# Optimization experiments

Measured on AMD Instinct MI355X. Metric: run time of the kernel, lower is better.

## Reference

```python
import jax, jax.numpy as jnp
import numpy as np

N, DIN, H, OUT = 2048, 128, 64, 7


def setup_inputs() -> dict:
    key = jax.random.key(0)
    ks = jax.random.split(key, 24)

    def lin(k, out_d, in_d):
        kw, kb = jax.random.split(k)
        s = 1.0 / np.sqrt(in_d)
        W = jax.random.uniform(kw, (out_d, in_d), minval=-s, maxval=s, dtype=jnp.float32)
        b = jax.random.uniform(kb, (out_d,), minval=-s, maxval=s, dtype=jnp.float32)
        return W, b

    x = jax.random.normal(ks[0], (N, DIN), dtype=jnp.float32)
    A = jax.random.uniform(ks[1], (N, N), dtype=jnp.float32)
    W1, b1 = lin(ks[2], H, DIN)
    WF1, bF1 = lin(ks[3], H, H)
    WF2, bF2 = lin(ks[4], H, H)
    WT1, bT1 = lin(ks[5], H, H)
    WT2, bT2 = lin(ks[6], H, H)
    WC1, bC1 = lin(ks[7], H, H)
    WC2, bC2 = lin(ks[8], H, H)
    Wa, ba = lin(ks[9], H, H)
    q = jax.random.normal(ks[10], (H,), dtype=jnp.float32)
    W2, b2 = lin(ks[11], OUT, H)
    return dict(x=x, A=A, k=4, W1=W1, b1=b1, WF1=WF1, bF1=bF1, WF2=WF2, bF2=bF2,
                WT1=WT1, bT1=bT1, WT2=WT2, bT2=bT2, WC1=WC1, bC1=bC1, WC2=WC2,
                bC2=bC2, Wa=Wa, ba=ba, q=q, W2=W2, b2=b2)


def leaky(x):
    return jnp.where(x > 0, x, 0.1 * x)


def laplacian(A):
    # D^{-1/2} A D^{-1/2} with diagonal D of (rowsum + 1e-10)
    d = (jnp.sum(A, -1) + 1e-10) ** -0.5
    return A * d[:, None] * d[None, :]


def cos_sim(x):
    n = jnp.sqrt(jnp.sum(x * x, -1, keepdims=True))
    s = x / n + 1e-10  # note: +1e-10 AFTER the division, as in the source
    return s @ s.T


def heat(x):
    # exp(-0.5 * sum_d ((x_i - x_j)^2 + 1e-10)); gram trick, same math as
    # the [d, N, N] broadcasted version in the source.
    sq = jnp.sum(x * x, -1)
    dist = sq[:, None] + sq[None, :] - 2.0 * (x @ x.T) + x.shape[-1] * 1e-10
    return jnp.exp(-0.5 * dist)


def l2_norm_rows(x):
    m = jnp.sqrt(jnp.mean(x * x, -1)) + 1e-10
    return x / m[:, None]


def hsic(x1, x2):
    n = x1.shape[-2]
    K1 = x1 @ x1.T
    K2 = x2 @ x2.T
    Rm = jnp.eye(n, dtype=x1.dtype) - jnp.ones((n, n), dtype=x1.dtype) / n
    P = Rm @ K1 @ Rm  # [N, N]
    # mean(I * (P @ K2)) * n^2/(n-1)^2 = trace(P @ K2)/(n-1)^2; K2 symmetric
    return jnp.sum(P * K2) / (n - 1) ** 2


def gnn(z, Ad, W, b):
    return leaky((Ad @ z) @ W.T + b)


def reference(x, A, k, W1, b1, WF1, bF1, WF2, bF2, WT1, bT1, WT2, bT2,
              WC1, bC1, WC2, bC2, Wa, ba, q, W2, b2):
    h = leaky(x @ W1.T + b1)                       # [N, H]
    At = laplacian(A)
    Hh = heat(h)                                    # [N, N]
    rank = jnp.argsort(jnp.argsort(-Hh, axis=-1), axis=-1)  # double-argsort rank
    mask = (rank < k).astype(h.dtype)
    Af = laplacian(cos_sim(h) * mask)
    zf = gnn(gnn(h, Af, WF1, bF1), Af, WF2, bF2)
    zt = gnn(gnn(h, At, WT1, bT1), At, WT2, bT2)
    zcf = gnn(gnn(h, Af, WC1, bC1), Af, WC2, bC2)
    zct = gnn(gnn(h, At, WC1, bC1), At, WC2, bC2)
    Lcf = l2_norm_rows(zcf)
    Lct = l2_norm_rows(zct)
    Lc = jnp.mean((Lcf @ Lcf.T - Lct @ Lct.T) ** 2)
    Ld = hsic(zt, zct) + hsic(zf, zcf)
    zc = (zcf + zct) / 2
    z = jnp.stack([zf, zt, zc], axis=-2)            # [N, 3, H]
    a = jax.nn.softmax(jnp.tanh(z @ Wa.T + ba) @ q, axis=-1)  # [N, 3]
    zagg = jnp.einsum('nkd,nk->nd', z, a)           # [N, H]
    out = zagg @ W2.T + b2                          # [N, OUT]
    return (out, Lc, Ld)
```

## Files before the change

### kernel.cpp

```cpp
#include <hip/hip_runtime.h>
#include <stdint.h>

#define N 2048
#define DIN 128
#define H 64
#define OUTD 7
#define RS 32
#define S1 8
#define S2 8

#define Z_ZT  0
#define Z_ZCT 64
#define Z_ZF  128
#define Z_ZCF 192
#define Z_LCF 256
#define Z_LCT 320

typedef short bf16x8 __attribute__((ext_vector_type(8)));
typedef float floatx4 __attribute__((ext_vector_type(4)));

__device__ __forceinline__ float leaky(float x){ return x > 0.f ? x : 0.1f*x; }

__device__ __forceinline__ unsigned short f2bf(float f){
  unsigned int u = __float_as_uint(f);
  u = u + 0x7FFFu + ((u >> 16) & 1u);
  return (unsigned short)(u >> 16);
}

__device__ __forceinline__ float waveRedSum(float v){
  #pragma unroll
  for (int o = 32; o > 0; o >>= 1) v += __shfl_xor(v, o, 64);
  return v;
}

__device__ __forceinline__ unsigned long long shflx64(unsigned long long v, int m){
  unsigned int lo = (unsigned int)v, hi = (unsigned int)(v >> 32);
  lo = (unsigned int)__shfl_xor((int)lo, m, 64);
  hi = (unsigned int)__shfl_xor((int)hi, m, 64);
  return ((unsigned long long)hi << 32) | lo;
}

__global__ void k_prep(const float* __restrict__ A, float* __restrict__ dA,
                       unsigned short* __restrict__ Abf){
  int i = blockIdx.x;
  const float4* row = (const float4*)(A + (size_t)i * N);
  unsigned short* ob = Abf + (size_t)i * N;
  float s = 0.f;
  #pragma unroll
  for (int it = 0; it < 2; it++){
    int u = threadIdx.x + it*256;
    float4 v = row[u];
    s += v.x + v.y + v.z + v.w;
    ushort4 o;
    o.x = f2bf(v.x); o.y = f2bf(v.y); o.z = f2bf(v.z); o.w = f2bf(v.w);
    *(ushort4*)&ob[u*4] = o;
  }
  __shared__ float red[4];
  s = waveRedSum(s);
  int wid = threadIdx.x >> 6, lane = threadIdx.x & 63;
  if (lane == 0) red[wid] = s;
  __syncthreads();
  if (threadIdx.x == 0){
    float t = red[0] + red[1] + red[2] + red[3];
    dA[i] = 1.0f / sqrtf(t + 1e-10f);
  }
}

__global__ void k_h(const float* __restrict__ x, const float* __restrict__ W1,
                    const float* __restrict__ b1, const float* __restrict__ dA,
                    float* __restrict__ h, unsigned short* __restrict__ hsT,
                    float* __restrict__ sq, float* __restrict__ hsum){
  int i = blockIdx.x, t = threadIdx.x;
  __shared__ float xr[DIN];
  xr[t]      = x[(size_t)i*DIN + t];
  xr[t + 64] = x[(size_t)i*DIN + t + 64];
  __syncthreads();
  float acc = b1[t];
  const float4* w  = (const float4*)(W1 + (size_t)t*DIN);
  const float4* xv = (const float4*)xr;
  #pragma unroll
  for (int c = 0; c < DIN/4; c++){
    float4 a = xv[c], b = w[c];
    acc += a.x*b.x + a.y*b.y + a.z*b.z + a.w*b.w;
  }
  float hv = leaky(acc);
  h[(size_t)i*H + t] = hv;
  hsT[(size_t)t*N + i] = f2bf(dA[i]*hv);
  float s2 = waveRedSum(hv*hv);
  float s1 = waveRedSum(hv);
  if (t == 0){ sq[i] = s2; hsum[i] = s1; }
}

__global__ __launch_bounds__(256) void k_gram(const float* __restrict__ h,
                                              float* __restrict__ DOT){
  __shared__ float at[32][132];
  __shared__ float bt[32][132];
  int bi = blockIdx.x, bj = blockIdx.y;
  int tid = threadIdx.x;
  int rg = tid >> 4, cg = tid & 15;
  float acc[8][8] = {};
  for (int kc = 0; kc < 64; kc += 32){
    for (int u = tid; u < 1024; u += 256){
      int row = u >> 3, k4 = u & 7;
      float4 v = *(const float4*)(h + (size_t)(bi*128 + row)*H + kc + k4*4);
      at[k4*4+0][row] = v.x; at[k4*4+1][row] = v.y;
      at[k4*4+2][row] = v.z; at[k4*4+3][row] = v.w;
    }
    for (int u = tid; u < 1024; u += 256){
      int row = u >> 3, k4 = u & 7;
      float4 v = *(const float4*)(h + (size_t)(bj*128 + row)*H + kc + k4*4);
      bt[k4*4+0][row] = v.x; bt[k4*4+1][row] = v.y;
      bt[k4*4+2][row] = v.z; bt[k4*4+3][row] = v.w;
    }
    __syncthreads();
    for (int k = 0; k < 32; k++){
      float a[8], b[8];
      *(float4*)&a[0] = *(const float4*)&at[k][rg*8];
      *(float4*)&a[4] = *(const float4*)&at[k][rg*8+4];
      *(float4*)&b[0] = *(const float4*)&bt[k][cg*8];
      *(float4*)&b[4] = *(const float4*)&bt[k][cg*8+4];
      #pragma unroll
      for (int ii = 0; ii < 8; ii++)
        #pragma unroll
        for (int jj = 0; jj < 8; jj++)
          acc[ii][jj] += a[ii]*b[jj];
    }
    __syncthreads();
  }
  #pragma unroll
  for (int ii = 0; ii < 8; ii++){
    int r = bi*128 + rg*8 + ii;
    float* out = DOT + (size_t)r*N + bj*128 + cg*8;
    *(float4*)(out)   = make_float4(acc[ii][0], acc[ii][1], acc[ii][2], acc[ii][3]);
    *(float4*)(out+4) = make_float4(acc[ii][4], acc[ii][5], acc[ii][6], acc[ii][7]);
  }
}

__global__ __launch_bounds__(256) void k_topk(const float* __restrict__ DOT,
      const float* __restrict__ sq, const float* __restrict__ hsum,
      int* __restrict__ nidx, float* __restrict__ ncos, float* __restrict__ df){
  int i = blockIdx.x, tid = threadIdx.x;
  __shared__ unsigned long long cand[1024];
  const float4* row = (const float4*)(DOT + (size_t)i * N);
  const float4* sq4 = (const float4*)sq;
  unsigned long long best[4] = {~0ULL, ~0ULL, ~0ULL, ~0ULL};
  #pragma unroll
  for (int blk = 0; blk < 2; blk++){
    int u = tid + blk*256;
    float4 d = row[u];
    float4 s = sq4[u];
    float kv[4] = { s.x - 2.f*d.x, s.y - 2.f*d.y, s.z - 2.f*d.z, s.w - 2.f*d.w };
    #pragma unroll
    for (int e = 0; e < 4; e++){
      unsigned int j = (unsigned int)(u*4 + e);
      unsigned int uk = __float_as_uint(kv[e]);
      uk = (uk & 0x80000000u) ? ~uk : (uk | 0x80000000u);
      unsigned long long c = ((unsigned long long)uk << 32) | j;
      if (c < best[3]){
        best[3] = c;
        unsigned long long t0;
        if (best[3] < best[2]){ t0 = best[2]; best[2] = best[3]; best[3] = t0; }
        if (best[2] < best[1]){ t0 = best[1]; best[1] = best[2]; best[2] = t0; }
        if (best[1] < best[0]){ t0 = best[0]; best[0] = best[1]; best[1] = t0; }
      }
    }
  }
  #pragma unroll
  for (int e = 0; e < 4; e++) cand[e*256 + tid] = best[e];
  __syncthreads();
  if (tid < 64){
    unsigned long long loc[16];
    #pragma unroll
    for (int e = 0; e < 16; e++) loc[e] = cand[e*64 + tid];
    unsigned long long w0=~0ULL, w1=~0ULL, w2=~0ULL, w3=~0ULL;
    #pragma unroll
    for (int r = 0; r < 4; r++){
      unsigned long long m = loc[0];
      #pragma unroll
      for (int e = 1; e < 16; e++) m = (loc[e] < m) ? loc[e] : m;
      unsigned long long g = m;
      #pragma unroll
      for (int o = 32; o > 0; o >>= 1){
        unsigned long long other = shflx64(g, o);
        if (other < g) g = other;
      }
      #pragma unroll
      for (int e = 0; e < 16; e++) if (loc[e] == g) loc[e] = ~0ULL;
      if (r == 0) w0 = g; else if (r == 1) w1 = g; else if (r == 2) w2 = g; else w3 = g;
    }
    float myc = 0.f;
    if (tid < 4){
      unsigned long long w = (tid==0) ? w0 : (tid==1) ? w1 : (tid==2) ? w2 : w3;
      unsigned int j = (unsigned int)w;
      unsigned int uk = (unsigned int)(w >> 32);
      float key = (uk & 0x80000000u) ? __uint_as_float(uk ^ 0x80000000u)
                                     : __uint_as_float(~uk);
      float sqj = sq[j];
      float dot = (sqj - key) * 0.5f;
      float hni = sqrtf(sq[i]), hnj = sqrtf(sqj);
      float cosv = dot/(hni*hnj)
                 + 1e-10f*(hsum[i]/hni + hsum[j]/hnj)
                 + 64.0f*1e-20f;
      nidx[i*4 + tid] = (int)j;
      ncos[i*4 + tid] = cosv;
      myc = cosv;
    }
    myc += __shfl_xor(myc, 1, 64);
    myc += __shfl_xor(myc, 2, 64);
    if (tid == 0) df[i] = 1.f / sqrtf(myc + 1e-10f);
  }
}

template<int BN>
__global__ __launch_bounds__(256) void k_mgemm(
    const unsigned short* __restrict__ Abf, const unsigned short* __restrict__ BtG,
    float* __restrict__ Cp, int KC){
  __shared__ __align__(16) unsigned short Asl[64][72];
  __shared__ __align__(16) unsigned short Bsl[BN][72];
  int m0 = blockIdx.x * 64, kbase = blockIdx.y * KC;
  int tid = threadIdx.x;
  int w = tid >> 6, lane = tid & 63;
  int quad = lane >> 4, ml = lane & 15;
  floatx4 acc[BN/16];
  #pragma unroll
  for (int ct = 0; ct < BN/16; ct++) acc[ct] = (floatx4){0.f,0.f,0.f,0.f};

  for (int kc = 0; kc < KC; kc += 64){
    int kb = kbase + kc;
    #pragma unroll
    for (int u = tid; u < 512; u += 256){
      int r = u >> 3, s = u & 7;
      *(uint4*)&Asl[r][s*8] = *(const uint4*)(Abf + ((size_t)(m0+r) << 11) + kb + s*8);
    }
    #pragma unroll
    for (int u = tid; u < BN*8; u += 256){
      int n = u >> 3, s = u & 7;
      *(uint4*)&Bsl[n][s*8] = *(const uint4*)(BtG + ((size_t)n << 11) + kb + s*8);
    }
    __syncthreads();
    #pragma unroll
    for (int k0 = 0; k0 < 64; k0 += 32){
      bf16x8 af = *(const bf16x8*)&Asl[16*w + ml][k0 + quad*8];
      #pragma unroll
      for (int ct = 0; ct < BN/16; ct++){
        bf16x8 bfr = *(const bf16x8*)&Bsl[16*ct + ml][k0 + quad*8];
        acc[ct] = __builtin_amdgcn_mfma_f32_16x16x32_bf16(af, bfr, acc[ct], 0, 0, 0);
      }
    }
    __syncthreads();
  }
  float* C = Cp + (size_t)blockIdx.y * (N * BN);
  #pragma unroll
  for (int ct = 0; ct < BN/16; ct++)
    #pragma unroll
    for (int r = 0; r < 4; r++){
      int row = m0 + 16*w + quad*4 + r;
      C[(size_t)row*BN + 16*ct + ml] = acc[ct][r];
    }
}

__global__ void k_z1(const float* __restrict__ h, const int* __restrict__ nidx,
                     const float* __restrict__ ncos, const float* __restrict__ df,
                     const float* __restrict__ Y1p, const float* __restrict__ dA,
                     const float* __restrict__ WF1, const float* __restrict__ bF1,
                     const float* __restrict__ WC1, const float* __restrict__ bC1,
                     const float* __restrict__ WT1, const float* __restrict__ bT1,
                     float* __restrict__ z1f, float* __restrict__ z1cf,
                     unsigned short* __restrict__ ZsT){
  int i = blockIdx.x, tid = threadIdx.x, w = tid >> 6, t = tid & 63;
  __shared__ float vu[2][H];
  if (w == 0){
    int j0 = nidx[i*4], j1 = nidx[i*4+1], j2 = nidx[i*4+2], j3 = nidx[i*4+3];
    float di = df[i];
    float w0 = ncos[i*4]  *di*df[j0];
    float w1 = ncos[i*4+1]*di*df[j1];
    float w2 = ncos[i*4+2]*di*df[j2];
    float w3 = ncos[i*4+3]*di*df[j3];
    vu[0][t] = w0*h[(size_t)j0*H+t] + w1*h[(size_t)j1*H+t]
             + w2*h[(size_t)j2*H+t] + w3*h[(size_t)j3*H+t];
  } else {
    float y = 0.f;
    #pragma unroll
    for (int p = 0; p < S1; p++) y += Y1p[(size_t)p*(N*H) + (size_t)i*H + t];
    vu[1][t] = dA[i] * y;
  }
  __syncthreads();
  const float* Wx = (w == 0) ? WF1 : WT1;
  const float* bx = (w == 0) ? bF1 : bT1;
  float a1 = bx[t], a2 = bC1[t];
  const float4* wx = (const float4*)(Wx + (size_t)t*H);
  const float4* wc = (const float4*)(WC1 + (size_t)t*H);
  const float4* vv = (const float4*)vu[w];
  #pragma unroll
  for (int c = 0; c < 16; c++){
    float4 x = vv[c], f = wx[c], g = wc[c];
    a1 += x.x*f.x + x.y*f.y + x.z*f.z + x.w*f.w;
    a2 += x.x*g.x + x.y*g.y + x.z*g.z + x.w*g.w;
  }
  if (w == 0){
    z1f [(size_t)i*H+t] = leaky(a1);
    z1cf[(size_t)i*H+t] = leaky(a2);
  } else {
    float di = dA[i];
    ZsT[(size_t)t*N + i]        = f2bf(di*leaky(a1));
    ZsT[(size_t)(64+t)*N + i]   = f2bf(di*leaky(a2));
  }
}

__global__ void k_z2o(const float* __restrict__ z1f, const float* __restrict__ z1cf,
                      const int* __restrict__ nidx, const float* __restrict__ ncos,
                      const float* __restrict__ df,
                      const float* __restrict__ Y2p, const float* __restrict__ dA,
                      const float* __restrict__ WF2, const float* __restrict__ bF2,
                      const float* __restrict__ WC2, const float* __restrict__ bC2,
                      const float* __restrict__ WT2, const float* __restrict__ bT2,
                      const float* __restrict__ Wa, const float* __restrict__ ba,
                      const float* __restrict__ q, const float* __restrict__ W2,
                      const float* __restrict__ b2,
                      float* __restrict__ Z6, float* __restrict__ out){
  int i = blockIdx.x, tid = threadIdx.x, w = tid >> 6, t = tid & 63;
  __shared__ float v[4][H];
  __shared__ float zsh[4][H];
  __shared__ float esh[3];
  __shared__ float zagg[H];
  if (w < 2){
    int j0 = nidx[i*4], j1 = nidx[i*4+1], j2 = nidx[i*4+2], j3 = nidx[i*4+3];
    float di = df[i];
    float w0 = ncos[i*4]  *di*df[j0];
    float w1 = ncos[i*4+1]*di*df[j1];
    float w2 = ncos[i*4+2]*di*df[j2];
    float w3 = ncos[i*4+3]*di*df[j3];
    const float* src = (w == 0) ? z1f : z1cf;
    v[w][t] = w0*src[(size_t)j0*H+t] + w1*src[(size_t)j1*H+t]
            + w2*src[(size_t)j2*H+t] + w3*src[(size_t)j3*H+t];
  } else {
    int off = (w == 2) ? 0 : 64;
    float y = 0.f;
    #pragma unroll
    for (int p = 0; p < S2; p++) y += Y2p[(size_t)p*(N*128) + (size_t)i*128 + off + t];
    v[w][t] = dA[i] * y;
  }
  __syncthreads();
  const float* WM = (w == 0) ? WF2 : (w == 2) ? WT2 : WC2;
  const float* bb = (w == 0) ? bF2 : (w == 2) ? bT2 : bC2;
  float a = bb[t];
  const float4* wm = (const float4*)(WM + (size_t)t*H);
  const float4* vv = (const float4*)v[w];
  #pragma unroll
  for (int c = 0; c < 16; c++){
    float4 x = vv[c], f = wm[c];
    a += x.x*f.x + x.y*f.y + x.z*f.z + x.w*f.w;
  }
  float val = leaky(a);
  float* zr = Z6 + (size_t)i*384;
  if (w == 0){
    zr[Z_ZF + t] = val;  zsh[0][t] = val;
  } else if (w == 2){
    zr[Z_ZT + t] = val;  zsh[1][t] = val;
  } else {
    int cf = (w == 1);
    zr[(cf ? Z_ZCF : Z_ZCT) + t] = val;
    zsh[cf ? 2 : 3][t] = val;
    float s = waveRedSum(val*val);
    float m = sqrtf(s*(1.f/64.f)) + 1e-10f;
    zr[(cf ? Z_LCF : Z_LCT) + t] = val/m;
  }
  __syncthreads();
  if (w < 3){
    float aa = ba[t];
    const float4* wa = (const float4*)(Wa + (size_t)t*H);
    const float4* z0 = (const float4*)zsh[w == 0 ? 0 : (w == 1 ? 1 : 2)];
    const float4* z3 = (const float4*)zsh[3];
    #pragma unroll
    for (int c = 0; c < 16; c++){
      float4 wv = wa[c];
      float4 zv = z0[c];
      if (w == 2){
        float4 z2v = z3[c];
        zv.x = 0.5f*(zv.x + z2v.x); zv.y = 0.5f*(zv.y + z2v.y);
        zv.z = 0.5f*(zv.z + z2v.z); zv.w = 0.5f*(zv.w + z2v.w);
      }
      aa += zv.x*wv.x + zv.y*wv.y + zv.z*wv.z + zv.w*wv.w;
    }
    float wk = tanhf(aa);
    float e = waveRedSum(wk*q[t]);
    if (t == 0) esh[w] = e;
  }
  __syncthreads();
  if (w == 3){
    float e0 = esh[0], e1 = esh[1], e2 = esh[2];
    float mx = fmaxf(e0, fmaxf(e1, e2));
    float x0 = expf(e0-mx), x1 = expf(e1-mx), x2 = expf(e2-mx);
    float inv = 1.f/(x0+x1+x2);
    float a0 = x0*inv, a1 = x1*inv, a2 = x2*inv;
    zagg[t] = a0*zsh[0][t] + a1*zsh[1][t] + a2*0.5f*(zsh[2][t] + zsh[3][t]);
    if (t < OUTD){
      float acc2 = b2[t];
      const float* w2r = W2 + (size_t)t*H;
      #pragma unroll
      for (int c = 0; c < H; c++) acc2 += zagg[c]*w2r[c];
      out[(size_t)i*OUTD + t] = acc2;
    }
  }
}

__global__ __launch_bounds__(256) void k_reduce(const float* __restrict__ Z6,
                                                float* __restrict__ redP,
                                                float* __restrict__ colP){
  __shared__ float sa[64][68];
  __shared__ float sb[64][68];
  int p = blockIdx.x >> 5;
  int s = blockIdx.x & 31;
  int tid = threadIdx.x;
  const int aoffT[5] = {Z_ZT,  Z_ZF,  Z_LCF, Z_LCF, Z_LCT};
  const int boffT[5] = {Z_ZCT, Z_ZCF, Z_LCF, Z_LCT, Z_LCT};
  int aoff = aoffT[p], boff = boffT[p];
  int r0 = s * 64;
  {
    int row = tid >> 4, c4 = (tid & 15) * 4;
    #pragma unroll
    for (int rr = 0; rr < 64; rr += 16){
      const float* zr = Z6 + (size_t)(r0 + row + rr) * 384;
      *(float4*)&sa[row + rr][c4] = *(const float4*)&zr[aoff + c4];
      *(float4*)&sb[row + rr][c4] = *(const float4*)&zr[boff + c4];
    }
  }
  __syncthreads();
  int rg = tid >> 4, cg = tid & 15;
  float acc[4][4] = {};
  #pragma unroll 8
  for (int k = 0; k < 64; k++){
    float a[4], b[4];
    *(float4*)a = *(const float4*)&sa[k][rg*4];
    *(float4*)b = *(const float4*)&sb[k][cg*4];
    #pragma unroll
    for (int ii = 0; ii < 4; ii++)
      #pragma unroll
      for (int jj = 0; jj < 4; jj++)
        acc[ii][jj] += a[ii]*b[jj];
  }
  float* rp = redP + (size_t)blockIdx.x * 4096;
  #pragma unroll
  for (int ii = 0; ii < 4; ii++)
    *(float4*)&rp[(rg*4+ii)*64 + cg*4] =
      make_float4(acc[ii][0], acc[ii][1], acc[ii][2], acc[ii][3]);
  if (p < 2 && tid < 128){
    int t = tid & 63;
    float csum = 0.f;
    if (tid < 64){
      #pragma unroll 16
      for (int r = 0; r < 64; r++) csum += sa[r][t];
    } else {
      #pragma unroll 16
      for (int r = 0; r < 64; r++) csum += sb[r][t];
    }
    colP[((size_t)p*RS + s)*128 + tid] = csum;
  }
}

__global__ void k_combine(const float* __restrict__ redP,
                          const float* __restrict__ colP,
                          float* __restrict__ red){
  int idx = blockIdx.x*256 + threadIdx.x;
  if (idx < 20480){
    int p = idx >> 12, i = idx & 4095;
    float sum = 0.f;
    #pragma unroll 8
    for (int s = 0; s < RS; s++) sum += redP[((size_t)p*RS + s)*4096 + i];
    red[idx] = sum;
  } else if (idx < 20736){
    int j = idx - 20480;
    int p = j >> 7, rem = j & 127;
    float sum = 0.f;
    #pragma unroll 8
    for (int s = 0; s < RS; s++) sum += colP[((size_t)p*RS + s)*128 + rem];
    red[idx] = sum;
  }
}

__global__ void k_final(const float* __restrict__ red, float* __restrict__ out2){
  int tid = threadIdx.x;
  const float* Stc = red;
  const float* Sfc = red + 4096;
  const float* Cff = red + 8192;
  const float* Cft = red + 12288;
  const float* Ctt = red + 16384;
  const float* cst = red + 20480;
  const float* csct= red + 20544;
  const float* csf = red + 20608;
  const float* cscf= red + 20672;
  float sCff=0, sCft=0, sCtt=0, sM1=0, sM2=0;
  for (int u = tid*16; u < tid*16+16; u++){
    int d = u >> 6, e = u & 63;
    float m1 = Stc[u] - cst[d]*csct[e]*(1.f/2048.f);
    float m2 = Sfc[u] - csf[d]*cscf[e]*(1.f/2048.f);
    sM1 += m1*m1; sM2 += m2*m2;
    float cf = Cff[u], cx = Cft[u], ct = Ctt[u];
    sCff += cf*cf; sCft += cx*cx; sCtt += ct*ct;
  }
  __shared__ float rd[5][4];
  sCff = waveRedSum(sCff); sCft = waveRedSum(sCft); sCtt = waveRedSum(sCtt);
  sM1 = waveRedSum(sM1);   sM2 = waveRedSum(sM2);
  int w = tid >> 6, lane = tid & 63;
  if (lane == 0){ rd[0][w]=sCff; rd[1][w]=sCft; rd[2][w]=sCtt; rd[3][w]=sM1; rd[4][w]=sM2; }
  __syncthreads();
  if (tid == 0){
    float A0 = rd[0][0]+rd[0][1]+rd[0][2]+rd[0][3];
    float A1 = rd[1][0]+rd[1][1]+rd[1][2]+rd[1][3];
    float A2 = rd[2][0]+rd[2][1]+rd[2][2]+rd[2][3];
    float M1 = rd[3][0]+rd[3][1]+rd[3][2]+rd[3][3];
    float M2 = rd[4][0]+rd[4][1]+rd[4][2]+rd[4][3];
    out2[0] = (A0 - 2.f*A1 + A2) * (1.f/(2048.f*2048.f));
    out2[1] = (M1 + M2) * (1.f/(2047.f*2047.f));
  }
}

extern "C" void kernel_launch(void* const* d_in, const int* in_sizes, int n_in,
                              void* d_out, int out_size, void* d_ws, size_t ws_size,
                              hipStream_t stream) {
  const float* x   = (const float*)d_in[0];
  const float* A   = (const float*)d_in[1];
  const float* W1  = (const float*)d_in[3];
  const float* b1  = (const float*)d_in[4];
  const float* WF1 = (const float*)d_in[5];
  const float* bF1 = (const float*)d_in[6];
  const float* WF2 = (const float*)d_in[7];
  const float* bF2 = (const float*)d_in[8];
  const float* WT1 = (const float*)d_in[9];
  const float* bT1 = (const float*)d_in[10];
  const float* WT2 = (const float*)d_in[11];
  const float* bT2 = (const float*)d_in[12];
  const float* WC1 = (const float*)d_in[13];
  const float* bC1 = (const float*)d_in[14];
  const float* WC2 = (const float*)d_in[15];
  const float* bC2 = (const float*)d_in[16];
  const float* Wa  = (const float*)d_in[17];
  const float* ba  = (const float*)d_in[18];
  const float* q   = (const float*)d_in[19];
  const float* W2  = (const float*)d_in[20];
  const float* b2  = (const float*)d_in[21];
  float* out = (float*)d_out;

  float* W = (float*)d_ws;
  float* h_   = W;
  float* dA   = h_  + N*H;
  float* sq   = dA  + N;
  float* hsum = sq  + N;
  float* df   = hsum+ N;
  int*   nidx = (int*)(df + N);
  float* ncos = (float*)(nidx + N*4);
  float* red  = ncos + N*4;
  float* DOT  = red + 20736;
  float* Z6   = DOT + (size_t)N*N;
  float* Y1p  = Z6  + (size_t)N*384;
  float* Y2p  = Y1p + (size_t)S1*N*H;
  float* z1f  = Y2p + (size_t)S2*N*128;
  float* z1cf = z1f + N*H;
  float* redP = z1cf+ N*H;
  float* colP = redP+ 655360;
  unsigned short* Abf = (unsigned short*)(colP + 8192);
  unsigned short* hsT = Abf + (size_t)N*N;
  unsigned short* ZsT = hsT + (size_t)H*N;

  k_prep<<<N, 256, 0, stream>>>(A, dA, Abf);
  k_h<<<N, 64, 0, stream>>>(x, W1, b1, dA, h_, hsT, sq, hsum);
  k_gram<<<dim3(16,16), 256, 0, stream>>>(h_, DOT);
  k_topk<<<N, 256, 0, stream>>>(DOT, sq, hsum, nidx, ncos, df);

  k_mgemm<64><<<dim3(32,S1), 256, 0, stream>>>(Abf, hsT, Y1p, N/S1);
  k_z1<<<N, 128, 0, stream>>>(h_, nidx, ncos, df, Y1p, dA,
                              WF1, bF1, WC1, bC1, WT1, bT1, z1f, z1cf, ZsT);
  k_mgemm<128><<<dim3(32,S2), 256, 0, stream>>>(Abf, ZsT, Y2p, N/S2);
  k_z2o<<<N, 256, 0, stream>>>(z1f, z1cf, nidx, ncos, df, Y2p, dA,
                               WF2, bF2, WC2, bC2, WT2, bT2,
                               Wa, ba, q, W2, b2, Z6, out);
  k_reduce<<<5*RS, 256, 0, stream>>>(Z6, redP, colP);
  k_combine<<<81, 256, 0, stream>>>(redP, colP, red);
  k_final<<<1, 256, 0, stream>>>(red, out + (size_t)N*OUTD);
}
```

Before: 235.3 us.

## Batch 16 rows per block in small dense kernels with LDS-staged weights

k_h, k_z1 and k_z2o now each handle 16 rows per 256-thread block, not one row per block. The weight matrices are loaded once into transposed, padded LDS and reused across those rows, instead of every row reading weights from global memory. The split-K partial sums from the mgemm stage are folded by new vectorised k_sumY1/k_sumY2 kernels, and the transposed bf16 outputs are staged in LDS so global stores are coalesced. The cost is two extra launches, only 128 blocks for a large GPU, and heavy LDS use that limits occupancy.

After: 232.6 us. No clear change (-1.2%).

```diff
diff --git a/kernel.cpp b/kernel.cpp
--- a/kernel.cpp
+++ b/kernel.cpp
@@ -66,29 +66,46 @@
   }
 }
 
-__global__ void k_h(const float* __restrict__ x, const float* __restrict__ W1,
-                    const float* __restrict__ b1, const float* __restrict__ dA,
+__global__ __launch_bounds__(256) void k_h(const float* __restrict__ x,
+                    const float* __restrict__ W1g, const float* __restrict__ b1,
+                    const float* __restrict__ dA,
                     float* __restrict__ h, unsigned short* __restrict__ hsT,
                     float* __restrict__ sq, float* __restrict__ hsum){
-  int i = blockIdx.x, t = threadIdx.x;
-  __shared__ float xr[DIN];
-  xr[t]      = x[(size_t)i*DIN + t];
-  xr[t + 64] = x[(size_t)i*DIN + t + 64];
-  __syncthreads();
-  float acc = b1[t];
-  const float4* w  = (const float4*)(W1 + (size_t)t*DIN);
-  const float4* xv = (const float4*)xr;
-  #pragma unroll
-  for (int c = 0; c < DIN/4; c++){
-    float4 a = xv[c], b = w[c];
-    acc += a.x*b.x + a.y*b.y + a.z*b.z + a.w*b.w;
-  }
-  float hv = leaky(acc);
-  h[(size_t)i*H + t] = hv;
-  hsT[(size_t)t*N + i] = f2bf(dA[i]*hv);
-  float s2 = waveRedSum(hv*hv);
-  float s1 = waveRedSum(hv);
-  if (t == 0){ sq[i] = s2; hsum[i] = s1; }
+  __shared__ float W1t[DIN][H+1];
+  __shared__ float xb[4][DIN];
+  __shared__ __align__(16) unsigned short hTb[H][16];
+  int tid = threadIdx.x, w = tid >> 6, t = tid & 63;
+  int i0 = blockIdx.x * 16;
+  for (int u = tid; u < 2048; u += 256){
+    float4 g = ((const float4*)W1g)[u];
+    int row = u >> 5, c0 = (u & 31) * 4;
+    W1t[c0+0][row] = g.x; W1t[c0+1][row] = g.y;
+    W1t[c0+2][row] = g.z; W1t[c0+3][row] = g.w;
+  }
+  __syncthreads();
+  float bt = b1[t];
+  for (int rr = 0; rr < 4; rr++){
+    int i = i0 + w*4 + rr;
+    xb[w][t]      = x[(size_t)i*DIN + t];
+    xb[w][t + 64] = x[(size_t)i*DIN + t + 64];
+    float acc = bt;
+    #pragma unroll
+    for (int c4 = 0; c4 < DIN/4; c4++){
+      float xv[4]; *(float4*)xv = *(const float4*)&xb[w][c4*4];
+      acc += xv[0]*W1t[c4*4+0][t] + xv[1]*W1t[c4*4+1][t]
+           + xv[2]*W1t[c4*4+2][t] + xv[3]*W1t[c4*4+3][t];
+    }
+    float hv = leaky(acc);
+    h[(size_t)i*H + t] = hv;
+    hTb[t][w*4+rr] = f2bf(dA[i]*hv);
+    float s2 = waveRedSum(hv*hv);
+    float s1 = waveRedSum(hv);
+    if (t == 0){ sq[i] = s2; hsum[i] = s1; }
+  }
+  __syncthreads();
+  { int c = tid >> 2, qq = tid & 3;
+    ushort4 v = *(ushort4*)&hTb[c][qq*4];
+    *(ushort4*)&hsT[(size_t)c*N + i0 + qq*4] = v; }
 }
 
 __global__ __launch_bounds__(256) void k_gram(const float* __restrict__ h,
@@ -259,146 +276,198 @@
     }
 }
 
-__global__ void k_z1(const float* __restrict__ h, const int* __restrict__ nidx,
-                     const float* __restrict__ ncos, const float* __restrict__ df,
-                     const float* __restrict__ Y1p, const float* __restrict__ dA,
-                     const float* __restrict__ WF1, const float* __restrict__ bF1,
-                     const float* __restrict__ WC1, const float* __restrict__ bC1,
-                     const float* __restrict__ WT1, const float* __restrict__ bT1,
+__global__ __launch_bounds__(256) void k_sumY1(const float* __restrict__ Y1p,
+    const float* __restrict__ dA, float* __restrict__ Y1s){
+  int idx4 = blockIdx.x*256 + threadIdx.x;
+  int i = idx4 >> 4;
+  float4 s = ((const float4*)Y1p)[idx4];
+  #pragma unroll
+  for (int p = 1; p < S1; p++){
+    float4 v = ((const float4*)Y1p)[(size_t)p*(N*H/4) + idx4];
+    s.x += v.x; s.y += v.y; s.z += v.z; s.w += v.w;
+  }
+  float d = dA[i];
+  s.x *= d; s.y *= d; s.z *= d; s.w *= d;
+  ((float4*)Y1s)[idx4] = s;
+}
+
+__global__ __launch_bounds__(256) void k_sumY2(const float* __restrict__ Y2p,
+    const float* __restrict__ dA, float* __restrict__ Y2s){
+  int idx4 = blockIdx.x*256 + threadIdx.x;
+  int i = idx4 >> 5;
+  float4 s = ((const float4*)Y2p)[idx4];
+  #pragma unroll
+  for (int p = 1; p < S2; p++){
+    float4 v = ((const float4*)Y2p)[(size_t)p*(N*128/4) + idx4];
+    s.x += v.x; s.y += v.y; s.z += v.z; s.w += v.w;
+  }
+  float d = dA[i];
+  s.x *= d; s.y *= d; s.z *= d; s.w *= d;
+  ((float4*)Y2s)[idx4] = s;
+}
+
+__global__ __launch_bounds__(256) void k_z1(const float* __restrict__ h,
+                     const int* __restrict__ nidx, const float* __restrict__ ncos,
+                     const float* __restrict__ df, const float* __restrict__ Y1s,
+                     const float* __restrict__ dA,
+                     const float* __restrict__ WF1g, const float* __restrict__ bF1,
+                     const float* __restrict__ WC1g, const float* __restrict__ bC1,
+                     const float* __restrict__ WT1g, const float* __restrict__ bT1,
                      float* __restrict__ z1f, float* __restrict__ z1cf,
                      unsigned short* __restrict__ ZsT){
-  int i = blockIdx.x, tid = threadIdx.x, w = tid >> 6, t = tid & 63;
-  __shared__ float vu[2][H];
-  if (w == 0){
+  __shared__ float Wf[H][H+1], Wc[H][H+1], Wt[H][H+1];
+  __shared__ float vb[4][H], ub[4][H];
+  __shared__ __align__(16) unsigned short Zb[128][16];
+  int tid = threadIdx.x, w = tid >> 6, t = tid & 63;
+  int i0 = blockIdx.x * 16;
+  for (int u = tid; u < 1024; u += 256){
+    int row = u >> 4, c0 = (u & 15) * 4;
+    float4 f = ((const float4*)WF1g)[u];
+    Wf[c0+0][row]=f.x; Wf[c0+1][row]=f.y; Wf[c0+2][row]=f.z; Wf[c0+3][row]=f.w;
+    float4 g = ((const float4*)WC1g)[u];
+    Wc[c0+0][row]=g.x; Wc[c0+1][row]=g.y; Wc[c0+2][row]=g.z; Wc[c0+3][row]=g.w;
+    float4 e = ((const float4*)WT1g)[u];
+    Wt[c0+0][row]=e.x; Wt[c0+1][row]=e.y; Wt[c0+2][row]=e.z; Wt[c0+3][row]=e.w;
+  }
+  __syncthreads();
+  float bfv = bF1[t], bcv = bC1[t], btv = bT1[t];
+  for (int rr = 0; rr < 4; rr++){
+    int i = i0 + w*4 + rr;
     int j0 = nidx[i*4], j1 = nidx[i*4+1], j2 = nidx[i*4+2], j3 = nidx[i*4+3];
     float di = df[i];
     float w0 = ncos[i*4]  *di*df[j0];
     float w1 = ncos[i*4+1]*di*df[j1];
     float w2 = ncos[i*4+2]*di*df[j2];
     float w3 = ncos[i*4+3]*di*df[j3];
-    vu[0][t] = w0*h[(size_t)j0*H+t] + w1*h[(size_t)j1*H+t]
+    vb[w][t] = w0*h[(size_t)j0*H+t] + w1*h[(size_t)j1*H+t]
              + w2*h[(size_t)j2*H+t] + w3*h[(size_t)j3*H+t];
-  } else {
-    float y = 0.f;
-    #pragma unroll
-    for (int p = 0; p < S1; p++) y += Y1p[(size_t)p*(N*H) + (size_t)i*H + t];
-    vu[1][t] = dA[i] * y;
-  }
-  __syncthreads();
-  const float* Wx = (w == 0) ? WF1 : WT1;
-  const float* bx = (w == 0) ? bF1 : bT1;
-  float a1 = bx[t], a2 = bC1[t];
-  const float4* wx = (const float4*)(Wx + (size_t)t*H);
-  const float4* wc = (const float4*)(WC1 + (size_t)t*H);
-  const float4* vv = (const float4*)vu[w];
-  #pragma unroll
-  for (int c = 0; c < 16; c++){
-    float4 x = vv[c], f = wx[c], g = wc[c];
-    a1 += x.x*f.x + x.y*f.y + x.z*f.z + x.w*f.w;
-    a2 += x.x*g.x + x.y*g.y + x.z*g.z + x.w*g.w;
-  }
-  if (w == 0){
+    ub[w][t] = Y1s[(size_t)i*H + t];
+    float a1 = bfv, a2 = bcv, a3 = btv, a4 = bcv;
+    #pragma unroll
+    for (int c4 = 0; c4 < 16; c4++){
+      float vv[4], uv[4];
+      *(float4*)vv = *(const float4*)&vb[w][c4*4];
+      *(float4*)uv = *(const float4*)&ub[w][c4*4];
+      #pragma unroll
+      for (int e = 0; e < 4; e++){
+        int c = c4*4 + e;
+        float wfv = Wf[c][t], wcv = Wc[c][t], wtv = Wt[c][t];
+        a1 += vv[e]*wfv; a2 += vv[e]*wcv;
+        a3 += uv[e]*wtv; a4 += uv[e]*wcv;
+      }
+    }
     z1f [(size_t)i*H+t] = leaky(a1);
     z1cf[(size_t)i*H+t] = leaky(a2);
-  } else {
-    float di = dA[i];
-    ZsT[(size_t)t*N + i]        = f2bf(di*leaky(a1));
-    ZsT[(size_t)(64+t)*N + i]   = f2bf(di*leaky(a2));
-  }
-}
-
-__global__ void k_z2o(const float* __restrict__ z1f, const float* __restrict__ z1cf,
+    float dai = dA[i];
+    int lr = w*4 + rr;
+    Zb[t][lr]      = f2bf(dai*leaky(a3));
+    Zb[64+t][lr]   = f2bf(dai*leaky(a4));
+  }
+  __syncthreads();
+  { int c = tid >> 1, hh = tid & 1;
+    uint4 v = *(uint4*)&Zb[c][hh*8];
+    *(uint4*)&ZsT[(size_t)c*N + i0 + hh*8] = v; }
+}
+
+__global__ __launch_bounds__(256) void k_z2o(const float* __restrict__ z1f,
+                      const float* __restrict__ z1cf,
                       const int* __restrict__ nidx, const float* __restrict__ ncos,
-                      const float* __restrict__ df,
-                      const float* __restrict__ Y2p, const float* __restrict__ dA,
-                      const float* __restrict__ WF2, const float* __restrict__ bF2,
-                      const float* __restrict__ WC2, const float* __restrict__ bC2,
-                      const float* __restrict__ WT2, const float* __restrict__ bT2,
-                      const float* __restrict__ Wa, const float* __restrict__ ba,
-                      const float* __restrict__ q, const float* __restrict__ W2,
+                      const float* __restrict__ df, const float* __restrict__ Y2s,
+                      const float* __restrict__ WF2g, const float* __restrict__ bF2,
+                      const float* __restrict__ WC2g, const float* __restrict__ bC2,
+                      const float* __restrict__ WT2g, const float* __restrict__ bT2,
+                      const float* __restrict__ Wag, const float* __restrict__ ba,
+                      const float* __restrict__ q,  const float* __restrict__ W2,
                       const float* __restrict__ b2,
                       float* __restrict__ Z6, float* __restrict__ out){
-  int i = blockIdx.x, tid = threadIdx.x, w = tid >> 6, t = tid & 63;
-  __shared__ float v[4][H];
-  __shared__ float zsh[4][H];
-  __shared__ float esh[3];
-  __shared__ float zagg[H];
-  if (w < 2){
+  __shared__ float Wf[H][H+1], Wc[H][H+1], Wt2[H][H+1], Wal[H][H+1];
+  __shared__ float vf[4][H], vc[4][H], ut[4][H], uc[4][H];
+  __shared__ float zfb[4][H], ztb[4][H], zcb[4][H], zab[4][H];
+  int tid = threadIdx.x, w = tid >> 6, t = tid & 63;
+  int i0 = blockIdx.x * 16;
+  for (int u = tid; u < 1024; u += 256){
+    int row = u >> 4, c0 = (u & 15) * 4;
+    float4 f = ((const float4*)WF2g)[u];
+    Wf[c0+0][row]=f.x; Wf[c0+1][row]=f.y; Wf[c0+2][row]=f.z; Wf[c0+3][row]=f.w;
+    float4 g = ((const float4*)WC2g)[u];
+    Wc[c0+0][row]=g.x; Wc[c0+1][row]=g.y; Wc[c0+2][row]=g.z; Wc[c0+3][row]=g.w;
+    float4 e = ((const float4*)WT2g)[u];
+    Wt2[c0+0][row]=e.x; Wt2[c0+1][row]=e.y; Wt2[c0+2][row]=e.z; Wt2[c0+3][row]=e.w;
+    float4 a = ((const float4*)Wag)[u];
+    Wal[c0+0][row]=a.x; Wal[c0+1][row]=a.y; Wal[c0+2][row]=a.z; Wal[c0+3][row]=a.w;
+  }
+  __syncthreads();
+  float bfv = bF2[t], bcv = bC2[t], btv = bT2[t];
+  float bav = ba[t], qv = q[t];
+  for (int rr = 0; rr < 4; rr++){
+    int i = i0 + w*4 + rr;
     int j0 = nidx[i*4], j1 = nidx[i*4+1], j2 = nidx[i*4+2], j3 = nidx[i*4+3];
     float di = df[i];
     float w0 = ncos[i*4]  *di*df[j0];
     float w1 = ncos[i*4+1]*di*df[j1];
     float w2 = ncos[i*4+2]*di*df[j2];
     float w3 = ncos[i*4+3]*di*df[j3];
-    const float* src = (w == 0) ? z1f : z1cf;
-    v[w][t] = w0*src[(size_t)j0*H+t] + w1*src[(size_t)j1*H+t]
-            + w2*src[(size_t)j2*H+t] + w3*src[(size_t)j3*H+t];
-  } else {
-    int off = (w == 2) ? 0 : 64;
-    float y = 0.f;
-    #pragma unroll
-    for (int p = 0; p < S2; p++) y += Y2p[(size_t)p*(N*128) + (size_t)i*128 + off + t];
-    v[w][t] = dA[i] * y;
-  }
-  __syncthreads();
-  const float* WM = (w == 0) ? WF2 : (w == 2) ? WT2 : WC2;
-  const float* bb = (w == 0) ? bF2 : (w == 2) ? bT2 : bC2;
-  float a = bb[t];
-  const float4* wm = (const float4*)(WM + (size_t)t*H);
-  const float4* vv = (const float4*)v[w];
-  #pragma unroll
-  for (int c = 0; c < 16; c++){
-    float4 x = vv[c], f = wm[c];
-    a += x.x*f.x + x.y*f.y + x.z*f.z + x.w*f.w;
-  }
-  float val = leaky(a);
-  float* zr = Z6 + (size_t)i*384;
-  if (w == 0){
-    zr[Z_ZF + t] = val;  zsh[0][t] = val;
-  } else if (w == 2){
-    zr[Z_ZT + t] = val;  zsh[1][t] = val;
-  } else {
-    int cf = (w == 1);
-    zr[(cf ? Z_ZCF : Z_ZCT) + t] = val;
-    zsh[cf ? 2 : 3][t] = val;
-    float s = waveRedSum(val*val);
-    float m = sqrtf(s*(1.f/64.f)) + 1e-10f;
-    zr[(cf ? Z_LCF : Z_LCT) + t] = val/m;
-  }
-  __syncthreads();
-  if (w < 3){
-    float aa = ba[t];
-    const float4* wa = (const float4*)(Wa + (size_t)t*H);
-    const float4* z0 = (const float4*)zsh[w == 0 ? 0 : (w == 1 ? 1 : 2)];
-    const float4* z3 = (const float4*)zsh[3];
-    #pragma unroll
-    for (int c = 0; c < 16; c++){
-      float4 wv = wa[c];
-      float4 zv = z0[c];
-      if (w == 2){
-        float4 z2v = z3[c];
-        zv.x = 0.5f*(zv.x + z2v.x); zv.y = 0.5f*(zv.y + z2v.y);
-        zv.z = 0.5f*(zv.z + z2v.z); zv.w = 0.5f*(zv.w + z2v.w);
+    vf[w][t] = w0*z1f[(size_t)j0*H+t] + w1*z1f[(size_t)j1*H+t]
+             + w2*z1f[(size_t)j2*H+t] + w3*z1f[(size_t)j3*H+t];
+    vc[w][t] = w0*z1cf[(size_t)j0*H+t] + w1*z1cf[(size_t)j1*H+t]
+             + w2*z1cf[(size_t)j2*H+t] + w3*z1cf[(size_t)j3*H+t];
+    ut[w][t] = Y2s[(size_t)i*128 + t];
+    uc[w][t] = Y2s[(size_t)i*128 + 64 + t];
+    float a1 = bfv, a2 = bcv, a3 = btv, a4 = bcv;
+    #pragma unroll
+    for (int c4 = 0; c4 < 16; c4++){
+      float fv[4], cv[4], tv[4], uv[4];
+      *(float4*)fv = *(const float4*)&vf[w][c4*4];
+      *(float4*)cv = *(const float4*)&vc[w][c4*4];
+      *(float4*)tv = *(const float4*)&ut[w][c4*4];
+      *(float4*)uv = *(const float4*)&uc[w][c4*4];
+      #pragma unroll
+      for (int e = 0; e < 4; e++){
+        int c = c4*4 + e;
+        float wfv = Wf[c][t], wcv = Wc[c][t], wtv = Wt2[c][t];
+        a1 += fv[e]*wfv; a2 += cv[e]*wcv;
+        a3 += tv[e]*wtv; a4 += uv[e]*wcv;
       }
-      aa += zv.x*wv.x + zv.y*wv.y + zv.z*wv.z + zv.w*wv.w;
-    }
-    float wk = tanhf(aa);
-    float e = waveRedSum(wk*q[t]);
-    if (t == 0) esh[w] = e;
-  }
-  __syncthreads();
-  if (w == 3){
-    float e0 = esh[0], e1 = esh[1], e2 = esh[2];
-    float mx = fmaxf(e0, fmaxf(e1, e2));
-    float x0 = expf(e0-mx), x1 = expf(e1-mx), x2 = expf(e2-mx);
+    }
+    float zfv = leaky(a1), zcfv = leaky(a2), ztv = leaky(a3), zctv = leaky(a4);
+    float* zr = Z6 + (size_t)i*384;
+    zr[Z_ZF + t] = zfv;  zr[Z_ZT + t] = ztv;
+    zr[Z_ZCF + t] = zcfv; zr[Z_ZCT + t] = zctv;
+    float scf = waveRedSum(zcfv*zcfv);
+    float mcf = sqrtf(scf*(1.f/64.f)) + 1e-10f;
+    zr[Z_LCF + t] = zcfv/mcf;
+    float sct = waveRedSum(zctv*zctv);
+    float mct = sqrtf(sct*(1.f/64.f)) + 1e-10f;
+    zr[Z_LCT + t] = zctv/mct;
+    float zcv = 0.5f*(zcfv + zctv);
+    zfb[w][t] = zfv; ztb[w][t] = ztv; zcb[w][t] = zcv;
+    float ev[3];
+    #pragma unroll
+    for (int kk = 0; kk < 3; kk++){
+      const float* zsrc = (kk == 0) ? zfb[w] : (kk == 1) ? ztb[w] : zcb[w];
+      float aa = bav;
+      #pragma unroll
+      for (int c4 = 0; c4 < 16; c4++){
+        float zv[4]; *(float4*)zv = *(const float4*)&zsrc[c4*4];
+        #pragma unroll
+        for (int e = 0; e < 4; e++) aa += zv[e]*Wal[c4*4+e][t];
+      }
+      ev[kk] = waveRedSum(tanhf(aa)*qv);
+    }
+    float mx = fmaxf(ev[0], fmaxf(ev[1], ev[2]));
+    float x0 = expf(ev[0]-mx), x1 = expf(ev[1]-mx), x2 = expf(ev[2]-mx);
     float inv = 1.f/(x0+x1+x2);
-    float a0 = x0*inv, a1 = x1*inv, a2 = x2*inv;
-    zagg[t] = a0*zsh[0][t] + a1*zsh[1][t] + a2*0.5f*(zsh[2][t] + zsh[3][t]);
+    float zagg = x0*inv*zfv + x1*inv*ztv + x2*inv*zcv;
+    zab[w][t] = zagg;
     if (t < OUTD){
       float acc2 = b2[t];
-      const float* w2r = W2 + (size_t)t*H;
-      #pragma unroll
-      for (int c = 0; c < H; c++) acc2 += zagg[c]*w2r[c];
+      const float4* w2r = (const float4*)(W2 + (size_t)t*H);
+      #pragma unroll
+      for (int c4 = 0; c4 < 16; c4++){
+        float4 wv = w2r[c4];
+        float zv[4]; *(float4*)zv = *(const float4*)&zab[w][c4*4];
+        acc2 += zv[0]*wv.x + zv[1]*wv.y + zv[2]*wv.z + zv[3]*wv.w;
+      }
       out[(size_t)i*OUTD + t] = acc2;
     }
   }
@@ -554,7 +623,9 @@
   float* Z6   = DOT + (size_t)N*N;
   float* Y1p  = Z6  + (size_t)N*384;
   float* Y2p  = Y1p + (size_t)S1*N*H;
-  float* z1f  = Y2p + (size_t)S2*N*128;
+  float* Y1s  = Y2p + (size_t)S2*N*128;
+  float* Y2s  = Y1s + (size_t)N*H;
+  float* z1f  = Y2s + (size_t)N*128;
   float* z1cf = z1f + N*H;
   float* redP = z1cf+ N*H;
   float* colP = redP+ 655360;
@@ -563,17 +634,19 @@
   unsigned short* ZsT = hsT + (size_t)H*N;
 
   k_prep<<<N, 256, 0, stream>>>(A, dA, Abf);
-  k_h<<<N, 64, 0, stream>>>(x, W1, b1, dA, h_, hsT, sq, hsum);
+  k_h<<<128, 256, 0, stream>>>(x, W1, b1, dA, h_, hsT, sq, hsum);
   k_gram<<<dim3(16,16), 256, 0, stream>>>(h_, DOT);
   k_topk<<<N, 256, 0, stream>>>(DOT, sq, hsum, nidx, ncos, df);
 
   k_mgemm<64><<<dim3(32,S1), 256, 0, stream>>>(Abf, hsT, Y1p, N/S1);
-  k_z1<<<N, 128, 0, stream>>>(h_, nidx, ncos, df, Y1p, dA,
-                              WF1, bF1, WC1, bC1, WT1, bT1, z1f, z1cf, ZsT);
+  k_sumY1<<<128, 256, 0, stream>>>(Y1p, dA, Y1s);
+  k_z1<<<128, 256, 0, stream>>>(h_, nidx, ncos, df, Y1s, dA,
+                                WF1, bF1, WC1, bC1, WT1, bT1, z1f, z1cf, ZsT);
   k_mgemm<128><<<dim3(32,S2), 256, 0, stream>>>(Abf, ZsT, Y2p, N/S2);
-  k_z2o<<<N, 256, 0, stream>>>(z1f, z1cf, nidx, ncos, df, Y2p, dA,
-                               WF2, bF2, WC2, bC2, WT2, bT2,
-                               Wa, ba, q, W2, b2, Z6, out);
+  k_sumY2<<<256, 256, 0, stream>>>(Y2p, dA, Y2s);
+  k_z2o<<<128, 256, 0, stream>>>(z1f, z1cf, nidx, ncos, df, Y2s,
+                                 WF2, bF2, WC2, bC2, WT2, bT2,
+                                 Wa, ba, q, W2, b2, Z6, out);
   k_reduce<<<5*RS, 256, 0, stream>>>(Z6, redP, colP);
   k_combine<<<81, 256, 0, stream>>>(redP, colP, red);
   k_final<<<1, 256, 0, stream>>>(red, out + (size_t)N*OUTD);
```
